# Performance work log

Hardware: AMD Instinct MI355X
Metric: run time of the kernel (lower is better)

The kernel has to match this reference:

```python
import jax, jax.numpy as jnp
import numpy as np

HID = 64
HEADS = 4
HEAD_DIM = HID // HEADS
N_MOL, N_PROT = 2048, 4096
E_MOL, E_PROT = 32768, 131072
B = 32


def _lin(key, din, dout):
    kw, kb = jax.random.split(key)
    s = 1.0 / np.sqrt(din)
    W = jax.random.uniform(kw, (din, dout), jnp.float32, -s, s)
    b = jax.random.uniform(kb, (dout,), jnp.float32, -s, s)
    return W, b


def setup_inputs() -> dict:
    key = jax.random.key(0)
    ks = jax.random.split(key, 32)
    inp = {}
    inp['mol_x'] = jax.random.normal(ks[0], (N_MOL, 11), jnp.float32)
    inp['prot_x'] = jax.random.normal(ks[1], (N_PROT, 15), jnp.float32)
    inp['mol_eattr'] = jax.random.normal(ks[2], (E_MOL, 10), jnp.float32)
    inp['prot_eattr'] = jax.random.normal(ks[3], (E_PROT, 10), jnp.float32)
    inp['mol_edge_index'] = jax.random.randint(ks[4], (2, E_MOL), 0, N_MOL, jnp.int32)
    inp['prot_edge_index'] = jax.random.randint(ks[5], (2, E_PROT), 0, N_PROT, jnp.int32)
    inp['mol_batch'] = jnp.sort(jax.random.randint(ks[6], (N_MOL,), 0, B, jnp.int32))
    inp['prot_batch'] = jnp.sort(jax.random.randint(ks[7], (N_PROT,), 0, B, jnp.int32))
    inp['node_lin_mol_W'], inp['node_lin_mol_b'] = _lin(ks[8], 11, HID)
    inp['node_lin_prot_W'], inp['node_lin_prot_b'] = _lin(ks[9], 15, HID)
    inp['edge_lin_mol_W'], inp['edge_lin_mol_b'] = _lin(ks[10], 10, HID)
    inp['edge_lin_prot_W'], inp['edge_lin_prot_b'] = _lin(ks[11], 10, HID)
    for pref, base in (('mol_conv', 12), ('prot_conv', 15)):
        W1s, b1s, W2s, b2s = [], [], [], []
        for l in range(3):
            k1, k2 = jax.random.split(ks[base + l])
            W1, b1 = _lin(k1, HID, HID)
            W2, b2 = _lin(k2, HID, HID)
            W1s.append(W1); b1s.append(b1); W2s.append(W2); b2s.append(b2)
        inp[pref + '_W1'] = jnp.stack(W1s); inp[pref + '_b1'] = jnp.stack(b1s)
        inp[pref + '_W2'] = jnp.stack(W2s); inp[pref + '_b2'] = jnp.stack(b2s)
    for pref, base in (('attn_mp', 18), ('attn_pm', 21)):
        Ws, bs = [], []
        for i in range(3):  # Q, K, V
            W, b = _lin(ks[base + i], HID, HID)
            Ws.append(W); bs.append(b)
        inp[pref + '_W'] = jnp.stack(Ws); inp[pref + '_b'] = jnp.stack(bs)
    inp['fc1_W'], inp['fc1_b'] = _lin(ks[24], 2 * HID, HID)
    inp['fc2_W'], inp['fc2_b'] = _lin(ks[25], HID, 1)
    return inp


def _gine_layer(x, src, dst, eattr, W1, b1, W2, b2):
    # message: ReLU(x_j + e_ji); GINEConv sum aggregation; eps = 0
    msg = jax.nn.relu(x[src] + eattr)                       # [E, H]
    agg = jax.ops.segment_sum(msg, dst, num_segments=x.shape[0])
    h = x + agg
    h = jax.nn.relu(h @ W1 + b1) @ W2 + b2                  # inner MLP
    return jax.nn.relu(h)                                   # post-conv ReLU


def _cross_attn(qn, kn, W, b):
    Nq, Nk = qn.shape[0], kn.shape[0]
    Q = (qn @ W[0] + b[0]).reshape(Nq, HEADS, HEAD_DIM)
    K = (kn @ W[1] + b[1]).reshape(Nk, HEADS, HEAD_DIM)
    V = (kn @ W[2] + b[2]).reshape(Nk, HEADS, HEAD_DIM)
    scores = jnp.einsum('qhd,khd->hqk', Q, K) / np.sqrt(HEAD_DIM)
    w = jax.nn.softmax(scores, axis=-1)
    out = jnp.einsum('hqk,khd->qhd', w, V)
    return out.reshape(Nq, HID)


def _pool(H, batch):
    s = jax.ops.segment_sum(H, batch, num_segments=B)
    c = jax.ops.segment_sum(jnp.ones((H.shape[0],), H.dtype), batch, num_segments=B)
    return s / jnp.maximum(c, 1.0)[:, None]


def _forward(mol_x, prot_x, mol_eattr, prot_eattr,
             node_lin_mol_W, node_lin_mol_b, node_lin_prot_W, node_lin_prot_b,
             edge_lin_mol_W, edge_lin_mol_b, edge_lin_prot_W, edge_lin_prot_b,
             mol_conv_W1, mol_conv_b1, mol_conv_W2, mol_conv_b2,
             prot_conv_W1, prot_conv_b1, prot_conv_W2, prot_conv_b2,
             attn_mp_W, attn_mp_b, attn_pm_W, attn_pm_b,
             fc1_W, fc1_b, fc2_W, fc2_b,
             mol_edge_index, prot_edge_index, mol_batch, prot_batch):
    xm = mol_x @ node_lin_mol_W + node_lin_mol_b
    xp = prot_x @ node_lin_prot_W + node_lin_prot_b
    em = mol_eattr @ edge_lin_mol_W + edge_lin_mol_b
    ep = prot_eattr @ edge_lin_prot_W + edge_lin_prot_b
    ms, md = mol_edge_index[0], mol_edge_index[1]
    ps, pd = prot_edge_index[0], prot_edge_index[1]
    for l in range(3):
        xm = _gine_layer(xm, ms, md, em, mol_conv_W1[l], mol_conv_b1[l], mol_conv_W2[l], mol_conv_b2[l])
    for l in range(3):
        xp = _gine_layer(xp, ps, pd, ep, prot_conv_W1[l], prot_conv_b1[l], prot_conv_W2[l], prot_conv_b2[l])
    H_mol = xm + _cross_attn(xm, xp, attn_mp_W, attn_mp_b)
    H_prot = xp + _cross_attn(xp, xm, attn_pm_W, attn_pm_b)
    z = jnp.concatenate([_pool(H_mol, mol_batch), _pool(H_prot, prot_batch)], axis=1)
    h = jax.nn.relu(z @ fc1_W + fc1_b)
    return jax.nn.sigmoid(h @ fc2_W + fc2_b).squeeze(-1)


def reference(mol_x, prot_x, mol_eattr, prot_eattr,
              node_lin_mol_W, node_lin_mol_b, node_lin_prot_W, node_lin_prot_b,
              edge_lin_mol_W, edge_lin_mol_b, edge_lin_prot_W, edge_lin_prot_b,
              mol_conv_W1, mol_conv_b1, mol_conv_W2, mol_conv_b2,
              prot_conv_W1, prot_conv_b1, prot_conv_W2, prot_conv_b2,
              attn_mp_W, attn_mp_b, attn_pm_W, attn_pm_b,
              fc1_W, fc1_b, fc2_W, fc2_b,
              mol_edge_index, prot_edge_index, mol_batch, prot_batch):
    return _forward(mol_x, prot_x, mol_eattr, prot_eattr,
                    node_lin_mol_W, node_lin_mol_b, node_lin_prot_W, node_lin_prot_b,
                    edge_lin_mol_W, edge_lin_mol_b, edge_lin_prot_W, edge_lin_prot_b,
                    mol_conv_W1, mol_conv_b1, mol_conv_W2, mol_conv_b2,
                    prot_conv_W1, prot_conv_b1, prot_conv_W2, prot_conv_b2,
                    attn_mp_W, attn_mp_b, attn_pm_W, attn_pm_b,
                    fc1_W, fc1_b, fc2_W, fc2_b,
                    mol_edge_index, prot_edge_index, mol_batch, prot_batch)
```

## Files before the change

### kernel.cpp

```cpp
#include <hip/hip_runtime.h>
#include <math.h>

#define HID 64
#define HEADS 4
#define HDIM 16
#define N_MOL 2048
#define N_PROT 4096
#define E_MOL 32768
#define E_PROT 131072
#define BATCH 32
#define N_TOT (N_MOL + N_PROT)
#define E_TOT (E_MOL + E_PROT)
#define CAP 128

#define TQA 16
#define TKA 32
#define KSTA 68
#define CH_MOL 4
#define CH_PROT 2
#define KCHUNK 1024
#define NGRP_MOL (N_MOL / TQA)

#define DOT4(a, b) ((a).x*(b).x + (a).y*(b).y + (a).z*(b).z + (a).w*(b).w)
#define EXP2(x) __builtin_amdgcn_exp2f(x)

__global__ void k_node_lin(const float* __restrict__ mol_x, const float* __restrict__ prot_x,
                           const float* __restrict__ Wm, const float* __restrict__ bm,
                           const float* __restrict__ Wp, const float* __restrict__ bp,
                           float* __restrict__ xm, float* __restrict__ xp) {
    int w = threadIdx.x >> 6, t = threadIdx.x & 63;
    int n = blockIdx.x * 4 + w;
    if (n < N_MOL) {
        const float* xr = mol_x + n * 11;
        float acc = bm[t];
#pragma unroll
        for (int i = 0; i < 11; ++i) acc += xr[i] * Wm[i * HID + t];
        xm[n * HID + t] = acc;
    } else {
        int p = n - N_MOL;
        const float* xr = prot_x + p * 15;
        float acc = bp[t];
#pragma unroll
        for (int i = 0; i < 15; ++i) acc += xr[i] * Wp[i * HID + t];
        xp[p * HID + t] = acc;
    }
}

__global__ void k_bucket(const int* __restrict__ mol_ei, const int* __restrict__ prot_ei,
                         int* __restrict__ cursor, int* __restrict__ eidx) {
    int e = blockIdx.x * 256 + threadIdx.x;
    int node, loc;
    if (e < E_MOL) { node = mol_ei[E_MOL + e]; loc = e; }
    else { int el = e - E_MOL; node = N_MOL + prot_ei[E_PROT + el]; loc = el; }
    int pos = atomicAdd(&cursor[node], 1);
    eidx[(size_t)node * CAP + pos] = loc;
}

__global__ void k_gine(const float* __restrict__ xin_m, const float* __restrict__ xin_p,
                       float* __restrict__ xout_m, float* __restrict__ xout_p,
                       const float* __restrict__ mol_ea, const float* __restrict__ prot_ea,
                       const int* __restrict__ mol_ei, const int* __restrict__ prot_ei,
                       const float* __restrict__ Wem, const float* __restrict__ bem,
                       const float* __restrict__ Wep, const float* __restrict__ bep,
                       const float* __restrict__ W1m, const float* __restrict__ b1m,
                       const float* __restrict__ W2m, const float* __restrict__ b2m,
                       const float* __restrict__ W1p, const float* __restrict__ b1p,
                       const float* __restrict__ W2p, const float* __restrict__ b2p,
                       const int* __restrict__ cnt, const int* __restrict__ eidx) {
    __shared__ float h0[8][HID];
    __shared__ float h1[8][HID];
    int w = threadIdx.x >> 6, t = threadIdx.x & 63;
    int nb0 = blockIdx.x * 8 + w * 2;
    bool isMol = nb0 < N_MOL;
    const float* x  = isMol ? xin_m : xin_p;
    float* xo       = isMol ? xout_m : xout_p;
    const float* We = isMol ? Wem : Wep;
    float bt        = isMol ? bem[t] : bep[t];
    const float* ea_base = isMol ? mol_ea : prot_ea;
    const int* srcarr    = isMol ? mol_ei : prot_ei;
    int nbias = isMol ? 0 : N_MOL;
    float wcol[10];
#pragma unroll
    for (int i = 0; i < 10; ++i) wcol[i] = We[i * HID + t];

#pragma unroll
    for (int u = 0; u < 2; ++u) {
        int nb = nb0 + u;
        int deg = cnt[nb];
        const int* lst = eidx + (size_t)nb * CAP;
        float agg = 0.f;
        int j = 0;
        for (; j + 1 < deg; j += 2) {
            int e0 = lst[j], e1 = lst[j + 1];
            int s0 = srcarr[e0], s1 = srcarr[e1];
            const float2* p0 = (const float2*)(ea_base + (size_t)e0 * 10);
            const float2* p1 = (const float2*)(ea_base + (size_t)e1 * 10);
            float2 a0 = p0[0], a1 = p0[1], a2 = p0[2], a3 = p0[3], a4 = p0[4];
            float2 c0 = p1[0], c1 = p1[1], c2 = p1[2], c3 = p1[3], c4 = p1[4];
            float xs0 = x[s0 * HID + t];
            float xs1 = x[s1 * HID + t];
            float m0 = bt, m1 = bt;
            m0 = fmaf(a0.x, wcol[0], m0); m0 = fmaf(a0.y, wcol[1], m0);
            m0 = fmaf(a1.x, wcol[2], m0); m0 = fmaf(a1.y, wcol[3], m0);
            m0 = fmaf(a2.x, wcol[4], m0); m0 = fmaf(a2.y, wcol[5], m0);
            m0 = fmaf(a3.x, wcol[6], m0); m0 = fmaf(a3.y, wcol[7], m0);
            m0 = fmaf(a4.x, wcol[8], m0); m0 = fmaf(a4.y, wcol[9], m0);
            m1 = fmaf(c0.x, wcol[0], m1); m1 = fmaf(c0.y, wcol[1], m1);
            m1 = fmaf(c1.x, wcol[2], m1); m1 = fmaf(c1.y, wcol[3], m1);
            m1 = fmaf(c2.x, wcol[4], m1); m1 = fmaf(c2.y, wcol[5], m1);
            m1 = fmaf(c3.x, wcol[6], m1); m1 = fmaf(c3.y, wcol[7], m1);
            m1 = fmaf(c4.x, wcol[8], m1); m1 = fmaf(c4.y, wcol[9], m1);
            agg += fmaxf(m0 + xs0, 0.f) + fmaxf(m1 + xs1, 0.f);
        }
        if (j < deg) {
            int e0 = lst[j];
            int s0 = srcarr[e0];
            const float2* p0 = (const float2*)(ea_base + (size_t)e0 * 10);
            float2 a0 = p0[0], a1 = p0[1], a2 = p0[2], a3 = p0[3], a4 = p0[4];
            float xs0 = x[s0 * HID + t];
            float m0 = bt;
            m0 = fmaf(a0.x, wcol[0], m0); m0 = fmaf(a0.y, wcol[1], m0);
            m0 = fmaf(a1.x, wcol[2], m0); m0 = fmaf(a1.y, wcol[3], m0);
            m0 = fmaf(a2.x, wcol[4], m0); m0 = fmaf(a2.y, wcol[5], m0);
            m0 = fmaf(a3.x, wcol[6], m0); m0 = fmaf(a3.y, wcol[7], m0);
            m0 = fmaf(a4.x, wcol[8], m0); m0 = fmaf(a4.y, wcol[9], m0);
            agg += fmaxf(m0 + xs0, 0.f);
        }
        h0[w * 2 + u][t] = x[(nb0 - nbias + u) * HID + t] + agg;
    }

    const float* W1 = isMol ? W1m : W1p;
    const float* W2 = isMol ? W2m : W2p;
    float b1v = isMol ? b1m[t] : b1p[t];
    float b2v = isMol ? b2m[t] : b2p[t];
    float acc0 = b1v, acc1 = b1v;
    const float4* hA = (const float4*)h0[w * 2];
    const float4* hB = (const float4*)h0[w * 2 + 1];
#pragma unroll
    for (int k = 0; k < 16; ++k) {
        float4 a = hA[k], b = hB[k];
        float w0 = W1[(4 * k + 0) * HID + t], w1 = W1[(4 * k + 1) * HID + t];
        float w2 = W1[(4 * k + 2) * HID + t], w3 = W1[(4 * k + 3) * HID + t];
        acc0 = fmaf(a.x, w0, acc0); acc1 = fmaf(b.x, w0, acc1);
        acc0 = fmaf(a.y, w1, acc0); acc1 = fmaf(b.y, w1, acc1);
        acc0 = fmaf(a.z, w2, acc0); acc1 = fmaf(b.z, w2, acc1);
        acc0 = fmaf(a.w, w3, acc0); acc1 = fmaf(b.w, w3, acc1);
    }
    h1[w * 2][t] = fmaxf(acc0, 0.f);
    h1[w * 2 + 1][t] = fmaxf(acc1, 0.f);
    float d0 = b2v, d1 = b2v;
    const float4* gA = (const float4*)h1[w * 2];
    const float4* gB = (const float4*)h1[w * 2 + 1];
#pragma unroll
    for (int k = 0; k < 16; ++k) {
        float4 a = gA[k], b = gB[k];
        float w0 = W2[(4 * k + 0) * HID + t], w1 = W2[(4 * k + 1) * HID + t];
        float w2 = W2[(4 * k + 2) * HID + t], w3 = W2[(4 * k + 3) * HID + t];
        d0 = fmaf(a.x, w0, d0); d1 = fmaf(b.x, w0, d1);
        d0 = fmaf(a.y, w1, d0); d1 = fmaf(b.y, w1, d1);
        d0 = fmaf(a.z, w2, d0); d1 = fmaf(b.z, w2, d1);
        d0 = fmaf(a.w, w3, d0); d1 = fmaf(b.w, w3, d1);
    }
    int n0 = nb0 - nbias;
    xo[n0 * HID + t] = fmaxf(d0, 0.f);
    xo[(n0 + 1) * HID + t] = fmaxf(d1, 0.f);
}

__global__ void k_qkv(const float* __restrict__ xm, const float* __restrict__ xp,
                      const float* __restrict__ mpW, const float* __restrict__ mpb,
                      const float* __restrict__ pmW, const float* __restrict__ pmb,
                      float* __restrict__ Qm, float* __restrict__ Kp, float* __restrict__ Vp,
                      float* __restrict__ Qp, float* __restrict__ Km, float* __restrict__ Vm) {
    __shared__ float row[8][HID];
    int w = threadIdx.x >> 6, t = threadIdx.x & 63;
    int b0 = blockIdx.x * 8;
    const float *src, *W, *bias;
    float* dst;
    int base;
    if (b0 < 2048)       { base = 0;     src = xm; W = mpW;        bias = mpb;       dst = Qm; }
    else if (b0 < 6144)  { base = 2048;  src = xp; W = mpW + 4096; bias = mpb + 64;  dst = Kp; }
    else if (b0 < 10240) { base = 6144;  src = xp; W = mpW + 8192; bias = mpb + 128; dst = Vp; }
    else if (b0 < 14336) { base = 10240; src = xp; W = pmW;        bias = pmb;       dst = Qp; }
    else if (b0 < 16384) { base = 14336; src = xm; W = pmW + 4096; bias = pmb + 64;  dst = Km; }
    else                 { base = 16384; src = xm; W = pmW + 8192; bias = pmb + 128; dst = Vm; }
    int n0 = b0 - base + w * 2, n1 = n0 + 1;
    row[w * 2][t] = src[n0 * HID + t];
    row[w * 2 + 1][t] = src[n1 * HID + t];
    float acc0 = bias[t], acc1 = acc0;
    const float4* rA = (const float4*)row[w * 2];
    const float4* rB = (const float4*)row[w * 2 + 1];
#pragma unroll
    for (int k = 0; k < 16; ++k) {
        float4 a = rA[k], b = rB[k];
        float w0 = W[(4 * k + 0) * HID + t], w1 = W[(4 * k + 1) * HID + t];
        float w2 = W[(4 * k + 2) * HID + t], w3 = W[(4 * k + 3) * HID + t];
        acc0 = fmaf(a.x, w0, acc0); acc1 = fmaf(b.x, w0, acc1);
        acc0 = fmaf(a.y, w1, acc0); acc1 = fmaf(b.y, w1, acc1);
        acc0 = fmaf(a.z, w2, acc0); acc1 = fmaf(b.z, w2, acc1);
        acc0 = fmaf(a.w, w3, acc0); acc1 = fmaf(b.w, w3, acc1);
    }
    dst[n0 * HID + t] = acc0;
    dst[n1 * HID + t] = acc1;
}

__device__ inline void upd4(float4& A, const float4 v0, const float4 v1,
                            float p0, float p1, float al) {
    A.x = fmaf(p1, v1.x, fmaf(p0, v0.x, A.x * al));
    A.y = fmaf(p1, v1.y, fmaf(p0, v0.y, A.y * al));
    A.z = fmaf(p1, v1.z, fmaf(p0, v0.z, A.z * al));
    A.w = fmaf(p1, v1.w, fmaf(p0, v0.w, A.w * al));
}

__device__ inline void merge4(float4& A, const float4 B, float c1, float c2) {
    A.x = A.x * c1 + B.x * c2;
    A.y = A.y * c1 + B.y * c2;
    A.z = A.z * c1 + B.z * c2;
    A.w = A.w * c1 + B.w * c2;
}

__device__ inline float4 shfl4(const float4 a, int off) {
    float4 r;
    r.x = __shfl_xor(a.x, off, 64); r.y = __shfl_xor(a.y, off, 64);
    r.z = __shfl_xor(a.z, off, 64); r.w = __shfl_xor(a.w, off, 64);
    return r;
}

__global__ __launch_bounds__(256) void k_attn(
    const float* __restrict__ Qm, const float* __restrict__ Kp, const float* __restrict__ Vp,
    const float* __restrict__ Qp, const float* __restrict__ Km, const float* __restrict__ Vm,
    float* __restrict__ part_m, float* __restrict__ part_p) {
    __shared__ float Kl[2][TKA * KSTA];
    __shared__ float Vl[2][TKA * KSTA];

    int t = threadIdx.x;
    const float *Q, *K, *V;
    float* part;
    int q0, chunk, CH;
    {
        int b = blockIdx.x;
        const int MOLB = NGRP_MOL * CH_MOL;
        if (b < MOLB) {
            chunk = b & 3; q0 = (b >> 2) * TQA; CH = CH_MOL;
            Q = Qm; K = Kp; V = Vp; part = part_m;
        } else {
            b -= MOLB;
            chunk = b & 1; q0 = (b >> 1) * TQA; CH = CH_PROT;
            Q = Qp; K = Km; V = Vm; part = part_p;
        }
    }
    int kbeg = chunk * KCHUNK;

    int sub = t & 15, h = (t >> 4) & 3, qg = t >> 6;
    int r0 = t >> 4;
    int c0 = (t & 15) << 2;

    const float sc = 0.25f * 1.44269504088896f;
    float4 q4[4][4];
#pragma unroll
    for (int qq = 0; qq < 4; ++qq) {
        const float4* Qr = (const float4*)(Q + (q0 + qg * 4 + qq) * HID + h * HDIM);
#pragma unroll
        for (int j = 0; j < 4; ++j) {
            float4 v = Qr[j];
            v.x *= sc; v.y *= sc; v.z *= sc; v.w *= sc;
            q4[qq][j] = v;
        }
    }

    float mreg[4], lreg[4];
    float4 A[4][4];
#pragma unroll
    for (int qq = 0; qq < 4; ++qq) {
        mreg[qq] = -INFINITY; lreg[qq] = 0.f;
#pragma unroll
        for (int j = 0; j < 4; ++j) A[qq][j] = (float4){0.f, 0.f, 0.f, 0.f};
    }

    {
        const float4* Kg = (const float4*)(K + kbeg * HID);
        const float4* Vg = (const float4*)(V + kbeg * HID);
        float4 ka = Kg[t], kb = Kg[t + 256];
        float4 va = Vg[t], vb = Vg[t + 256];
        *(float4*)&Kl[0][r0 * KSTA + c0] = ka;
        *(float4*)&Kl[0][(r0 + 16) * KSTA + c0] = kb;
        *(float4*)&Vl[0][r0 * KSTA + c0] = va;
        *(float4*)&Vl[0][(r0 + 16) * KSTA + c0] = vb;
    }
    __syncthreads();

    const int NT = KCHUNK / TKA;
    for (int tile = 0; tile < NT; ++tile) {
        int cur = tile & 1;
        float4 ka, kb, va, vb;
        bool more = (tile + 1) < NT;
        if (more) {
            const float4* Kg = (const float4*)(K + (kbeg + (tile + 1) * TKA) * HID);
            const float4* Vg = (const float4*)(V + (kbeg + (tile + 1) * TKA) * HID);
            ka = Kg[t]; kb = Kg[t + 256];
            va = Vg[t]; vb = Vg[t + 256];
        }

        const float4* Kr0 = (const float4*)&Kl[cur][sub * KSTA + h * HDIM];
        const float4* Kr1 = (const float4*)&Kl[cur][(sub + 16) * KSTA + h * HDIM];
        float4 x0 = Kr0[0], x1 = Kr0[1], x2 = Kr0[2], x3 = Kr0[3];
        float4 y0 = Kr1[0], y1 = Kr1[1], y2 = Kr1[2], y3 = Kr1[3];

        float s0[4], s1[4];
#pragma unroll
        for (int qq = 0; qq < 4; ++qq) {
            s0[qq] = DOT4(x0, q4[qq][0]) + DOT4(x1, q4[qq][1]) + DOT4(x2, q4[qq][2]) + DOT4(x3, q4[qq][3]);
            s1[qq] = DOT4(y0, q4[qq][0]) + DOT4(y1, q4[qq][1]) + DOT4(y2, q4[qq][2]) + DOT4(y3, q4[qq][3]);
        }

        const float4* Vr0 = (const float4*)&Vl[cur][sub * KSTA + h * HDIM];
        const float4* Vr1 = (const float4*)&Vl[cur][(sub + 16) * KSTA + h * HDIM];
        float4 v00 = Vr0[0], v01 = Vr0[1], v02 = Vr0[2], v03 = Vr0[3];
        float4 v10 = Vr1[0], v11 = Vr1[1], v12 = Vr1[2], v13 = Vr1[3];

#pragma unroll
        for (int qq = 0; qq < 4; ++qq) {
            float mn = fmaxf(mreg[qq], fmaxf(s0[qq], s1[qq]));
            float al = EXP2(mreg[qq] - mn);
            float p0 = EXP2(s0[qq] - mn);
            float p1 = EXP2(s1[qq] - mn);
            lreg[qq] = lreg[qq] * al + p0 + p1;
            upd4(A[qq][0], v00, v10, p0, p1, al);
            upd4(A[qq][1], v01, v11, p0, p1, al);
            upd4(A[qq][2], v02, v12, p0, p1, al);
            upd4(A[qq][3], v03, v13, p0, p1, al);
            mreg[qq] = mn;
        }

        if (more) {
            int nxt = cur ^ 1;
            *(float4*)&Kl[nxt][r0 * KSTA + c0] = ka;
            *(float4*)&Kl[nxt][(r0 + 16) * KSTA + c0] = kb;
            *(float4*)&Vl[nxt][r0 * KSTA + c0] = va;
            *(float4*)&Vl[nxt][(r0 + 16) * KSTA + c0] = vb;
        }
        __syncthreads();
    }

#pragma unroll
    for (int off = 1; off < 16; off <<= 1) {
#pragma unroll
        for (int qq = 0; qq < 4; ++qq) {
            float m2 = __shfl_xor(mreg[qq], off, 64);
            float l2 = __shfl_xor(lreg[qq], off, 64);
            float4 B0 = shfl4(A[qq][0], off), B1 = shfl4(A[qq][1], off);
            float4 B2 = shfl4(A[qq][2], off), B3 = shfl4(A[qq][3], off);
            float mn = fmaxf(mreg[qq], m2);
            float c1 = EXP2(mreg[qq] - mn), c2 = EXP2(m2 - mn);
            lreg[qq] = lreg[qq] * c1 + l2 * c2;
            merge4(A[qq][0], B0, c1, c2); merge4(A[qq][1], B1, c1, c2);
            merge4(A[qq][2], B2, c1, c2); merge4(A[qq][3], B3, c1, c2);
            mreg[qq] = mn;
        }
    }

    if (sub == 0) {
#pragma unroll
        for (int qq = 0; qq < 4; ++qq) {
            int qi = q0 + qg * 4 + qq;
            float* pp = part + (size_t)((qi * HEADS + h) * CH + chunk) * 20;
            pp[0] = mreg[qq]; pp[1] = lreg[qq];
            *(float4*)&pp[4] = A[qq][0]; *(float4*)&pp[8] = A[qq][1];
            *(float4*)&pp[12] = A[qq][2]; *(float4*)&pp[16] = A[qq][3];
        }
    }
}

__global__ void k_attn_merge(const float* __restrict__ part_m, const float* __restrict__ part_p,
                             const float* __restrict__ xm, const float* __restrict__ xp,
                             float* __restrict__ Hm, float* __restrict__ Hp) {
    int gi = blockIdx.x * 256 + threadIdx.x;
    const float *part, *X;
    float* H;
    int CH;
    if (gi < N_MOL * HEADS) { part = part_m; X = xm; H = Hm; CH = CH_MOL; }
    else { gi -= N_MOL * HEADS; part = part_p; X = xp; H = Hp; CH = CH_PROT; }
    int q = gi >> 2, h = gi & 3;
    const float* p0 = part + (size_t)gi * CH * 20;
    float mmax = -INFINITY;
    for (int c = 0; c < CH; ++c) mmax = fmaxf(mmax, p0[c * 20]);
    float lsum = 0.f, wgt[4];
    for (int c = 0; c < CH; ++c) {
        wgt[c] = EXP2(p0[c * 20] - mmax);
        lsum += p0[c * 20 + 1] * wgt[c];
    }
    float inv = 1.f / lsum;
    const float4* Xr = (const float4*)(X + q * HID + h * HDIM);
    float4* Hr = (float4*)(H + q * HID + h * HDIM);
#pragma unroll
    for (int j = 0; j < 4; ++j) {
        float4 o = Xr[j];
        for (int c = 0; c < CH; ++c) {
            const float4 Av = *(const float4*)(p0 + c * 20 + 4 + 4 * j);
            float wc = wgt[c] * inv;
            o.x += Av.x * wc; o.y += Av.y * wc; o.z += Av.z * wc; o.w += Av.w * wc;
        }
        Hr[j] = o;
    }
}

__global__ void k_poolfinal(const float* __restrict__ Hm, const float* __restrict__ Hp,
                            const int* __restrict__ mb, const int* __restrict__ pb,
                            const float* __restrict__ fc1W, const float* __restrict__ fc1b,
                            const float* __restrict__ fc2W, const float* __restrict__ fc2b,
                            float* __restrict__ out) {
    __shared__ float part[4][HID];
    __shared__ float z[2 * HID];
    int b = blockIdx.x;
    int t = threadIdx.x;
    int col = t & 63, w = t >> 6;
    int ms, me, ps, pe;
    {
        int lo = 0, hi = N_MOL;
        while (lo < hi) { int mid = (lo + hi) >> 1; if (mb[mid] < b) lo = mid + 1; else hi = mid; }
        ms = lo; lo = ms; hi = N_MOL;
        while (lo < hi) { int mid = (lo + hi) >> 1; if (mb[mid] < b + 1) lo = mid + 1; else hi = mid; }
        me = lo;
        lo = 0; hi = N_PROT;
        while (lo < hi) { int mid = (lo + hi) >> 1; if (pb[mid] < b) lo = mid + 1; else hi = mid; }
        ps = lo; lo = ps; hi = N_PROT;
        while (lo < hi) { int mid = (lo + hi) >> 1; if (pb[mid] < b + 1) lo = mid + 1; else hi = mid; }
        pe = lo;
    }
    float s = 0.f;
    if (w < 2) {
        for (int r = ms + w; r < me; r += 2) s += Hm[r * HID + col];
    } else {
        for (int r = ps + (w - 2); r < pe; r += 2) s += Hp[r * HID + col];
    }
    part[w][col] = s;
    __syncthreads();
    if (w == 0) z[col] = (part[0][col] + part[1][col]) / fmaxf((float)(me - ms), 1.f);
    else if (w == 1) z[64 + col] = (part[2][col] + part[3][col]) / fmaxf((float)(pe - ps), 1.f);
    __syncthreads();
    if (t < 64) {
        float acc = fc1b[t];
        const float4* zv = (const float4*)z;
#pragma unroll
        for (int k = 0; k < 32; ++k) {
            float4 hv = zv[k];
            acc = fmaf(hv.x, fc1W[(4 * k + 0) * 64 + t], acc);
            acc = fmaf(hv.y, fc1W[(4 * k + 1) * 64 + t], acc);
            acc = fmaf(hv.z, fc1W[(4 * k + 2) * 64 + t], acc);
            acc = fmaf(hv.w, fc1W[(4 * k + 3) * 64 + t], acc);
        }
        float hv = fmaxf(acc, 0.f);
        float prod = hv * fc2W[t];
#pragma unroll
        for (int off = 32; off > 0; off >>= 1) prod += __shfl_xor(prod, off, 64);
        if (t == 0) out[b] = 1.f / (1.f + __expf(-(prod + fc2b[0])));
    }
}

extern "C" void kernel_launch(void* const* d_in, const int* in_sizes, int n_in,
                              void* d_out, int out_size, void* d_ws, size_t ws_size,
                              hipStream_t stream) {
    const float* mol_x   = (const float*)d_in[0];
    const float* prot_x  = (const float*)d_in[1];
    const float* mol_ea  = (const float*)d_in[2];
    const float* prot_ea = (const float*)d_in[3];
    const int*   mol_ei  = (const int*)d_in[4];
    const int*   prot_ei = (const int*)d_in[5];
    const int*   mol_b   = (const int*)d_in[6];
    const int*   prot_b  = (const int*)d_in[7];
    const float* nlmW = (const float*)d_in[8];
    const float* nlmb = (const float*)d_in[9];
    const float* nlpW = (const float*)d_in[10];
    const float* nlpb = (const float*)d_in[11];
    const float* elmW = (const float*)d_in[12];
    const float* elmb = (const float*)d_in[13];
    const float* elpW = (const float*)d_in[14];
    const float* elpb = (const float*)d_in[15];
    const float* mcW1 = (const float*)d_in[16];
    const float* mcb1 = (const float*)d_in[17];
    const float* mcW2 = (const float*)d_in[18];
    const float* mcb2 = (const float*)d_in[19];
    const float* pcW1 = (const float*)d_in[20];
    const float* pcb1 = (const float*)d_in[21];
    const float* pcW2 = (const float*)d_in[22];
    const float* pcb2 = (const float*)d_in[23];
    const float* mpW  = (const float*)d_in[24];
    const float* mpb  = (const float*)d_in[25];
    const float* pmW  = (const float*)d_in[26];
    const float* pmb  = (const float*)d_in[27];
    const float* fc1W = (const float*)d_in[28];
    const float* fc1b = (const float*)d_in[29];
    const float* fc2W = (const float*)d_in[30];
    const float* fc2b = (const float*)d_in[31];

    float* ws    = (float*)d_ws;
    float* xa_m  = ws;
    float* xa_p  = xa_m + 131072;
    float* xb_m  = xa_p + 262144;
    float* xb_p  = xb_m + 131072;
    float* Qm    = xb_p + 262144;
    float* Kp    = Qm + 131072;
    float* Vp    = Kp + 262144;
    float* Qp    = Vp + 262144;
    float* Km    = Qp + 262144;
    float* Vm    = Km + 131072;
    float* partm = Vm + 131072;
    float* partp = partm + 655360;
    int* cursor  = (int*)(partp + 655360);
    int* eidx    = (int*)partm;
    float* Hm = Qm;
    float* Hp = Qp;

    hipMemsetAsync(cursor, 0, (size_t)N_TOT * 4, stream);

    k_node_lin<<<N_TOT / 4, 256, 0, stream>>>(mol_x, prot_x, nlmW, nlmb, nlpW, nlpb, xa_m, xa_p);
    k_bucket<<<E_TOT / 256, 256, 0, stream>>>(mol_ei, prot_ei, cursor, eidx);

    k_gine<<<N_TOT / 8, 256, 0, stream>>>(xa_m, xa_p, xb_m, xb_p, mol_ea, prot_ea, mol_ei, prot_ei,
        elmW, elmb, elpW, elpb,
        mcW1, mcb1, mcW2, mcb2, pcW1, pcb1, pcW2, pcb2, cursor, eidx);
    k_gine<<<N_TOT / 8, 256, 0, stream>>>(xb_m, xb_p, xa_m, xa_p, mol_ea, prot_ea, mol_ei, prot_ei,
        elmW, elmb, elpW, elpb,
        mcW1 + 4096, mcb1 + 64, mcW2 + 4096, mcb2 + 64,
        pcW1 + 4096, pcb1 + 64, pcW2 + 4096, pcb2 + 64, cursor, eidx);
    k_gine<<<N_TOT / 8, 256, 0, stream>>>(xa_m, xa_p, xb_m, xb_p, mol_ea, prot_ea, mol_ei, prot_ei,
        elmW, elmb, elpW, elpb,
        mcW1 + 8192, mcb1 + 128, mcW2 + 8192, mcb2 + 128,
        pcW1 + 8192, pcb1 + 128, pcW2 + 8192, pcb2 + 128, cursor, eidx);

    k_qkv<<<18432 / 8, 256, 0, stream>>>(xb_m, xb_p, mpW, mpb, pmW, pmb, Qm, Kp, Vp, Qp, Km, Vm);
    k_attn<<<NGRP_MOL * CH_MOL + (N_PROT / TQA) * CH_PROT, 256, 0, stream>>>(
        Qm, Kp, Vp, Qp, Km, Vm, partm, partp);
    k_attn_merge<<<(N_MOL + N_PROT) * HEADS / 256, 256, 0, stream>>>(
        partm, partp, xb_m, xb_p, Hm, Hp);

    k_poolfinal<<<BATCH, 256, 0, stream>>>(Hm, Hp, mol_b, prot_b,
                                           fc1W, fc1b, fc2W, fc2b, (float*)d_out);
}
```

Measured before the change: 394.8 us.

## Fuse attention merge into pooling, merge node-lin with bucketing, split mol keys finer

Combines the node linear and edge bucketing kernels into one launch, and folds the per-head softmax partial merge directly into the per-graph pooling and final MLP kernel. This removes the intermediate H buffers and two launches. Mol-side attention is split into 8 key chunks instead of 4 to raise parallelism. The cost is a larger partials buffer and merge work concentrated in only 32 blocks.

```diff
diff --git a/kernel.cpp b/kernel.cpp
--- a/kernel.cpp
+++ b/kernel.cpp
@@ -16,44 +16,44 @@
 #define TQA 16
 #define TKA 32
 #define KSTA 68
-#define CH_MOL 4
+#define CH_MOL 8
 #define CH_PROT 2
-#define KCHUNK 1024
 #define NGRP_MOL (N_MOL / TQA)
 
 #define DOT4(a, b) ((a).x*(b).x + (a).y*(b).y + (a).z*(b).z + (a).w*(b).w)
 #define EXP2(x) __builtin_amdgcn_exp2f(x)
 
-__global__ void k_node_lin(const float* __restrict__ mol_x, const float* __restrict__ prot_x,
-                           const float* __restrict__ Wm, const float* __restrict__ bm,
-                           const float* __restrict__ Wp, const float* __restrict__ bp,
-                           float* __restrict__ xm, float* __restrict__ xp) {
-    int w = threadIdx.x >> 6, t = threadIdx.x & 63;
-    int n = blockIdx.x * 4 + w;
-    if (n < N_MOL) {
-        const float* xr = mol_x + n * 11;
-        float acc = bm[t];
-#pragma unroll
-        for (int i = 0; i < 11; ++i) acc += xr[i] * Wm[i * HID + t];
-        xm[n * HID + t] = acc;
+__global__ void k_nlb(const float* __restrict__ mol_x, const float* __restrict__ prot_x,
+                      const float* __restrict__ Wm, const float* __restrict__ bm,
+                      const float* __restrict__ Wp, const float* __restrict__ bp,
+                      const int* __restrict__ mol_ei, const int* __restrict__ prot_ei,
+                      float* __restrict__ xm, float* __restrict__ xp,
+                      int* __restrict__ cursor, int* __restrict__ eidx) {
+    if (blockIdx.x < N_TOT / 4) {
+        int w = threadIdx.x >> 6, t = threadIdx.x & 63;
+        int n = blockIdx.x * 4 + w;
+        if (n < N_MOL) {
+            const float* xr = mol_x + n * 11;
+            float acc = bm[t];
+#pragma unroll
+            for (int i = 0; i < 11; ++i) acc += xr[i] * Wm[i * HID + t];
+            xm[n * HID + t] = acc;
+        } else {
+            int p = n - N_MOL;
+            const float* xr = prot_x + p * 15;
+            float acc = bp[t];
+#pragma unroll
+            for (int i = 0; i < 15; ++i) acc += xr[i] * Wp[i * HID + t];
+            xp[p * HID + t] = acc;
+        }
     } else {
-        int p = n - N_MOL;
-        const float* xr = prot_x + p * 15;
-        float acc = bp[t];
-#pragma unroll
-        for (int i = 0; i < 15; ++i) acc += xr[i] * Wp[i * HID + t];
-        xp[p * HID + t] = acc;
-    }
-}
-
-__global__ void k_bucket(const int* __restrict__ mol_ei, const int* __restrict__ prot_ei,
-                         int* __restrict__ cursor, int* __restrict__ eidx) {
-    int e = blockIdx.x * 256 + threadIdx.x;
-    int node, loc;
-    if (e < E_MOL) { node = mol_ei[E_MOL + e]; loc = e; }
-    else { int el = e - E_MOL; node = N_MOL + prot_ei[E_PROT + el]; loc = el; }
-    int pos = atomicAdd(&cursor[node], 1);
-    eidx[(size_t)node * CAP + pos] = loc;
+        int e = (blockIdx.x - N_TOT / 4) * 256 + threadIdx.x;
+        int node, loc;
+        if (e < E_MOL) { node = mol_ei[E_MOL + e]; loc = e; }
+        else { int el = e - E_MOL; node = N_MOL + prot_ei[E_PROT + el]; loc = el; }
+        int pos = atomicAdd(&cursor[node], 1);
+        eidx[(size_t)node * CAP + pos] = loc;
+    }
 }
 
 __global__ void k_gine(const float* __restrict__ xin_m, const float* __restrict__ xin_p,
@@ -235,20 +235,20 @@
     int t = threadIdx.x;
     const float *Q, *K, *V;
     float* part;
-    int q0, chunk, CH;
+    int q0, chunk, CH, KC;
     {
         int b = blockIdx.x;
         const int MOLB = NGRP_MOL * CH_MOL;
         if (b < MOLB) {
-            chunk = b & 3; q0 = (b >> 2) * TQA; CH = CH_MOL;
+            chunk = b & 7; q0 = (b >> 3) * TQA; CH = CH_MOL; KC = N_PROT / CH_MOL;
             Q = Qm; K = Kp; V = Vp; part = part_m;
         } else {
             b -= MOLB;
-            chunk = b & 1; q0 = (b >> 1) * TQA; CH = CH_PROT;
+            chunk = b & 1; q0 = (b >> 1) * TQA; CH = CH_PROT; KC = N_MOL / CH_PROT;
             Q = Qp; K = Km; V = Vm; part = part_p;
         }
     }
-    int kbeg = chunk * KCHUNK;
+    int kbeg = chunk * KC;
 
     int sub = t & 15, h = (t >> 4) & 3, qg = t >> 6;
     int r0 = t >> 4;
@@ -288,7 +288,7 @@
     }
     __syncthreads();
 
-    const int NT = KCHUNK / TKA;
+    const int NT = KC / TKA;
     for (int tile = 0; tile < NT; ++tile) {
         int cur = tile & 1;
         float4 ka, kb, va, vb;
@@ -370,49 +370,17 @@
     }
 }
 
-__global__ void k_attn_merge(const float* __restrict__ part_m, const float* __restrict__ part_p,
-                             const float* __restrict__ xm, const float* __restrict__ xp,
-                             float* __restrict__ Hm, float* __restrict__ Hp) {
-    int gi = blockIdx.x * 256 + threadIdx.x;
-    const float *part, *X;
-    float* H;
-    int CH;
-    if (gi < N_MOL * HEADS) { part = part_m; X = xm; H = Hm; CH = CH_MOL; }
-    else { gi -= N_MOL * HEADS; part = part_p; X = xp; H = Hp; CH = CH_PROT; }
-    int q = gi >> 2, h = gi & 3;
-    const float* p0 = part + (size_t)gi * CH * 20;
-    float mmax = -INFINITY;
-    for (int c = 0; c < CH; ++c) mmax = fmaxf(mmax, p0[c * 20]);
-    float lsum = 0.f, wgt[4];
-    for (int c = 0; c < CH; ++c) {
-        wgt[c] = EXP2(p0[c * 20] - mmax);
-        lsum += p0[c * 20 + 1] * wgt[c];
-    }
-    float inv = 1.f / lsum;
-    const float4* Xr = (const float4*)(X + q * HID + h * HDIM);
-    float4* Hr = (float4*)(H + q * HID + h * HDIM);
-#pragma unroll
-    for (int j = 0; j < 4; ++j) {
-        float4 o = Xr[j];
-        for (int c = 0; c < CH; ++c) {
-            const float4 Av = *(const float4*)(p0 + c * 20 + 4 + 4 * j);
-            float wc = wgt[c] * inv;
-            o.x += Av.x * wc; o.y += Av.y * wc; o.z += Av.z * wc; o.w += Av.w * wc;
-        }
-        Hr[j] = o;
-    }
-}
-
-__global__ void k_poolfinal(const float* __restrict__ Hm, const float* __restrict__ Hp,
-                            const int* __restrict__ mb, const int* __restrict__ pb,
-                            const float* __restrict__ fc1W, const float* __restrict__ fc1b,
-                            const float* __restrict__ fc2W, const float* __restrict__ fc2b,
-                            float* __restrict__ out) {
-    __shared__ float part[4][HID];
+__global__ void k_final(const float* __restrict__ part_m, const float* __restrict__ part_p,
+                        const float* __restrict__ xm, const float* __restrict__ xp,
+                        const int* __restrict__ mb, const int* __restrict__ pb,
+                        const float* __restrict__ fc1W, const float* __restrict__ fc1b,
+                        const float* __restrict__ fc2W, const float* __restrict__ fc2b,
+                        float* __restrict__ out) {
+    __shared__ float sm[64][65];
     __shared__ float z[2 * HID];
     int b = blockIdx.x;
     int t = threadIdx.x;
-    int col = t & 63, w = t >> 6;
+    int h = t & 3, s = t >> 2;
     int ms, me, ps, pe;
     {
         int lo = 0, hi = N_MOL;
@@ -426,17 +394,71 @@
         while (lo < hi) { int mid = (lo + hi) >> 1; if (pb[mid] < b + 1) lo = mid + 1; else hi = mid; }
         pe = lo;
     }
-    float s = 0.f;
-    if (w < 2) {
-        for (int r = ms + w; r < me; r += 2) s += Hm[r * HID + col];
-    } else {
-        for (int r = ps + (w - 2); r < pe; r += 2) s += Hp[r * HID + col];
-    }
-    part[w][col] = s;
+
+    {
+        float acc[16];
+#pragma unroll
+        for (int d = 0; d < 16; ++d) acc[d] = 0.f;
+        for (int q = ms + s; q < me; q += 64) {
+            const float* p0 = part_m + (size_t)(q * HEADS + h) * CH_MOL * 20;
+            float mmax = -INFINITY;
+#pragma unroll
+            for (int c = 0; c < CH_MOL; ++c) mmax = fmaxf(mmax, p0[c * 20]);
+            float lsum = 0.f, wgt[CH_MOL];
+#pragma unroll
+            for (int c = 0; c < CH_MOL; ++c) {
+                wgt[c] = EXP2(p0[c * 20] - mmax);
+                lsum += p0[c * 20 + 1] * wgt[c];
+            }
+            float inv = 1.f / lsum;
+            const float* Xr = xm + q * HID + h * HDIM;
+#pragma unroll
+            for (int d = 0; d < 16; ++d) {
+                float o = Xr[d];
+#pragma unroll
+                for (int c = 0; c < CH_MOL; ++c)
+                    o = fmaf(p0[c * 20 + 4 + d], wgt[c] * inv, o);
+                acc[d] += o;
+            }
+        }
+#pragma unroll
+        for (int d = 0; d < 16; ++d) sm[s][h * 16 + d] = acc[d];
+    }
     __syncthreads();
-    if (w == 0) z[col] = (part[0][col] + part[1][col]) / fmaxf((float)(me - ms), 1.f);
-    else if (w == 1) z[64 + col] = (part[2][col] + part[3][col]) / fmaxf((float)(pe - ps), 1.f);
+    if (t < 64) {
+        float sum = 0.f;
+        for (int ss = 0; ss < 64; ++ss) sum += sm[ss][t];
+        z[t] = sum / fmaxf((float)(me - ms), 1.f);
+    }
     __syncthreads();
+
+    {
+        float acc[16];
+#pragma unroll
+        for (int d = 0; d < 16; ++d) acc[d] = 0.f;
+        for (int q = ps + s; q < pe; q += 64) {
+            const float* p0 = part_p + (size_t)(q * HEADS + h) * CH_PROT * 20;
+            float m0 = p0[0], m1 = p0[20];
+            float mmax = fmaxf(m0, m1);
+            float w0 = EXP2(m0 - mmax), w1 = EXP2(m1 - mmax);
+            float inv = 1.f / (p0[1] * w0 + p0[21] * w1);
+            w0 *= inv; w1 *= inv;
+            const float* Xr = xp + q * HID + h * HDIM;
+#pragma unroll
+            for (int d = 0; d < 16; ++d)
+                acc[d] += Xr[d] + p0[4 + d] * w0 + p0[24 + d] * w1;
+        }
+#pragma unroll
+        for (int d = 0; d < 16; ++d) sm[s][h * 16 + d] = acc[d];
+    }
+    __syncthreads();
+    if (t < 64) {
+        float sum = 0.f;
+        for (int ss = 0; ss < 64; ++ss) sum += sm[ss][t];
+        z[64 + t] = sum / fmaxf((float)(pe - ps), 1.f);
+    }
+    __syncthreads();
+
     if (t < 64) {
         float acc = fc1b[t];
         const float4* zv = (const float4*)z;
@@ -504,16 +526,14 @@
     float* Km    = Qp + 262144;
     float* Vm    = Km + 131072;
     float* partm = Vm + 131072;
-    float* partp = partm + 655360;
+    float* partp = partm + 1310720;
     int* cursor  = (int*)(partp + 655360);
     int* eidx    = (int*)partm;
-    float* Hm = Qm;
-    float* Hp = Qp;
 
     hipMemsetAsync(cursor, 0, (size_t)N_TOT * 4, stream);
 
-    k_node_lin<<<N_TOT / 4, 256, 0, stream>>>(mol_x, prot_x, nlmW, nlmb, nlpW, nlpb, xa_m, xa_p);
-    k_bucket<<<E_TOT / 256, 256, 0, stream>>>(mol_ei, prot_ei, cursor, eidx);
+    k_nlb<<<N_TOT / 4 + E_TOT / 256, 256, 0, stream>>>(
+        mol_x, prot_x, nlmW, nlmb, nlpW, nlpb, mol_ei, prot_ei, xa_m, xa_p, cursor, eidx);
 
     k_gine<<<N_TOT / 8, 256, 0, stream>>>(xa_m, xa_p, xb_m, xb_p, mol_ea, prot_ea, mol_ei, prot_ei,
         elmW, elmb, elpW, elpb,
@@ -530,9 +550,7 @@
     k_qkv<<<18432 / 8, 256, 0, stream>>>(xb_m, xb_p, mpW, mpb, pmW, pmb, Qm, Kp, Vp, Qp, Km, Vm);
     k_attn<<<NGRP_MOL * CH_MOL + (N_PROT / TQA) * CH_PROT, 256, 0, stream>>>(
         Qm, Kp, Vp, Qp, Km, Vm, partm, partp);
-    k_attn_merge<<<(N_MOL + N_PROT) * HEADS / 256, 256, 0, stream>>>(
-        partm, partp, xb_m, xb_p, Hm, Hp);
-
-    k_poolfinal<<<BATCH, 256, 0, stream>>>(Hm, Hp, mol_b, prot_b,
-                                           fc1W, fc1b, fc2W, fc2b, (float*)d_out);
-}
+
+    k_final<<<BATCH, 256, 0, stream>>>(partm, partp, xb_m, xb_p, mol_b, prot_b,
+                                       fc1W, fc1b, fc2W, fc2b, (float*)d_out);
+}
```

Result: faster. 385.4 us (-2.4%).
